# Optimization experiments

Measured on AMD Instinct MI355X. Metric: run time of the kernel, lower is better.

## Reference

```python
import jax, jax.numpy as jnp
import numpy as np

KERNEL_SIZES = [2, 4, 8, 16, 32, 64]
MAXK = max(k + k // 2 for k in KERNEL_SIZES[1:])  # 96
PAD_LO = (MAXK - 1) // 2  # 47
PAD_HI = MAXK - 1 - PAD_LO  # 48


def _alternating(K, even_negative):
    f = np.ones(K, np.float32)
    idx = np.arange(K)
    mask = (idx % 2 == 0) if even_negative else (idx % 2 == 1)
    f[mask] = -1.0
    return f


def make_weight_bank():
    """Builds all 17 fixed filters, zero-padded and center-aligned into one
    (17, 1, MAXK) bank so a single 'same'-padded conv matches 17 torch convs.
    Alignment: torch pads left=(K-1)//2 for kernel K; embedding each kernel at
    offset (MAXK-1)//2 - (K-1)//2 inside a MAXK kernel padded (PAD_LO, PAD_HI)
    reproduces the identical output."""
    filters = []
    for K in KERNEL_SIZES:              # group 1: -1 at even indices
        filters.append(_alternating(K, True))
    for K in KERNEL_SIZES:              # group 2: -1 at odd indices
        filters.append(_alternating(K, False))
    for K in KERNEL_SIZES[1:]:          # group 3: piecewise quadratic, len K + K//2
        q = K // 4
        left = (np.linspace(0.0, 1.0, q + 1, dtype=np.float32)[1:]) ** 2
        right = left[::-1]
        filters.append(np.concatenate([-left, -right, 2 * left, 2 * right, -left, -right]).astype(np.float32))
    W = np.zeros((len(filters), 1, MAXK), np.float32)
    for i, f in enumerate(filters):
        K = len(f)
        o = (MAXK - 1) // 2 - (K - 1) // 2
        W[i, 0, o:o + K] = f
    return jnp.asarray(W)


def setup_inputs() -> dict:
    key = jax.random.key(0)
    x = jax.random.normal(key, (128, 1, 32768), dtype=jnp.float32)
    W = make_weight_bank()  # (17, 1, 96), fixed non-trainable filters
    return {"x": x, "W": W}


def reference(x, W):
    # x: (B, 1, L); W: (17, 1, MAXK). One cross-correlation conv = bank of 17
    # 'same'-padded conv1d filters; then ReLU.
    y = jax.lax.conv_general_dilated(
        x, W,
        window_strides=(1,),
        padding=[(PAD_LO, PAD_HI)],
        dimension_numbers=("NCH", "OIH", "NCH"),
    )
    return jax.nn.relu(y)  # (B, 17, L)
```

## Files before the change

### kernel.cpp

```cpp
#include <hip/hip_runtime.h>


#define S_LEN   32768
#define NFILT   17
#define TILE    1024
#define HALO_L  47
#define WIN     (TILE + 96)
#define NCHUNK  (WIN / 8)
#define PITCH   284
#define NTHREADS 256

template<int Q>
__device__ __forceinline__ float third_w(int j) {
    constexpr float inv = 1.0f / (float)Q;
    const int seg = j / Q;
    const int i = j - seg * Q;
    const float t = (seg == 0 || seg == 2 || seg == 4) ? (float)(i + 1) * inv
                                                       : (float)(Q - i) * inv;
    const float v = t * t;
    return (seg == 2 || seg == 3) ? 2.0f * v : -v;
}

template<int K>
__device__ __forceinline__ float4 third_acc(const float* __restrict__ xsp, int tid) {
    constexpr int Q    = K / 4;
    constexpr int SPAN = 6 * Q;
    constexpr int C    = (3 * K / 2 - 1) / 2;
    float a0 = 0.f, a1 = 0.f, a2 = 0.f, a3 = 0.f;
#pragma unroll
    for (int u = 0; u < SPAN + 3; ++u) {
        const int d = (HALO_L - C) + u;
        const float xv = xsp[(d & 3) * PITCH + tid + (d >> 2)];
        if (u < SPAN)               a0 = fmaf(third_w<Q>(u),     xv, a0);
        if (u >= 1 && u - 1 < SPAN) a1 = fmaf(third_w<Q>(u - 1), xv, a1);
        if (u >= 2 && u - 2 < SPAN) a2 = fmaf(third_w<Q>(u - 2), xv, a2);
        if (u >= 3 && u - 3 < SPAN) a3 = fmaf(third_w<Q>(u - 3), xv, a3);
    }
    return make_float4(a0, a1, a2, a3);
}

template<int K>
__device__ __forceinline__ float4 alt_acc(const float* __restrict__ Qsp, int tid) {
    constexpr int H = (K - 1) / 2;
    float v[4];
#pragma unroll
    for (int r = 0; r < 4; ++r) {
        const int d  = HALO_L + r - H;
        const int d2 = d + K;
        const float qa = Qsp[(d  & 3) * PITCH + tid + (d  >> 2)];
        const float qb = Qsp[(d2 & 3) * PITCH + tid + (d2 >> 2)];
        const float dd = qb - qa;
        v[r] = (d & 1) ? dd : -dd;
    }
    return make_float4(v[0], v[1], v[2], v[3]);
}

__global__ __launch_bounds__(NTHREADS)
void conv_bank_kernel(const float* __restrict__ x, float* __restrict__ out) {
    __shared__ float xsp[4 * PITCH];
    __shared__ float Qsp[4 * PITCH];
    __shared__ float scanb[NTHREADS];

    const int tid = threadIdx.x;
    const int ts  = blockIdx.x * TILE;
    const int b   = blockIdx.y;
    const float* __restrict__ xrow = x + (size_t)b * S_LEN;

    for (int j = tid; j < WIN; j += NTHREADS) {
        const int g = ts - HALO_L + j;
        float v = 0.f;
        if ((unsigned)g < (unsigned)S_LEN) v = xrow[g];
        xsp[(j & 3) * PITCH + (j >> 2)] = v;
    }
    __syncthreads();

    float csum = 0.f;
    if (tid < NCHUNK) {
#pragma unroll
        for (int k = 0; k < 8; ++k) {
            const float v = xsp[(k & 3) * PITCH + 2 * tid + (k >> 2)];
            csum += (k & 1) ? -v : v;
        }
    }
    scanb[tid] = csum;
    __syncthreads();
    float incl = csum;
#pragma unroll
    for (int off = 1; off < NTHREADS; off <<= 1) {
        const float add = (tid >= off) ? scanb[tid - off] : 0.f;
        __syncthreads();
        incl += add;
        scanb[tid] = incl;
        __syncthreads();
    }
    if (tid < NCHUNK) {
        float run = incl - csum;
#pragma unroll
        for (int k = 0; k < 8; ++k) {
            const int idx = (k & 3) * PITCH + 2 * tid + (k >> 2);
            Qsp[idx] = run;
            const float v = xsp[idx];
            run += (k & 1) ? -v : v;
        }
        if (tid == NCHUNK - 1) Qsp[WIN >> 2] = run;
    }
    __syncthreads();

    const int t0 = ts + 4 * tid;
    float* __restrict__ obase = out + (size_t)b * NFILT * S_LEN + t0;

    auto store_relu = [&](int j, float4 v) {
        float4 s;
        s.x = fmaxf(v.x, 0.f); s.y = fmaxf(v.y, 0.f);
        s.z = fmaxf(v.z, 0.f); s.w = fmaxf(v.w, 0.f);
        *reinterpret_cast<float4*>(obase + (size_t)j * S_LEN) = s;
    };
    auto store_pair = [&](int j, float4 a) {
        store_relu(j, a);
        store_relu(j + 6, make_float4(-a.x, -a.y, -a.z, -a.w));
    };

    store_pair(0, alt_acc<2 >(Qsp, tid));
    store_pair(1, alt_acc<4 >(Qsp, tid));
    store_pair(2, alt_acc<8 >(Qsp, tid));
    store_pair(3, alt_acc<16>(Qsp, tid));
    store_pair(4, alt_acc<32>(Qsp, tid));
    store_pair(5, alt_acc<64>(Qsp, tid));

    store_relu(12, third_acc<4 >(xsp, tid));
    store_relu(13, third_acc<8 >(xsp, tid));
    store_relu(14, third_acc<16>(xsp, tid));
    store_relu(15, third_acc<32>(xsp, tid));
    store_relu(16, third_acc<64>(xsp, tid));
}

extern "C" void kernel_launch(void* const* d_in, const int* in_sizes, int n_in,
                              void* d_out, int out_size, void* d_ws, size_t ws_size,
                              hipStream_t stream) {
    const float* x = (const float*)d_in[0];
    float* out = (float*)d_out;
    const int nbatch = in_sizes[0] / S_LEN;
    dim3 grid(S_LEN / TILE, nbatch, 1);
    conv_bank_kernel<<<grid, NTHREADS, 0, stream>>>(x, out);
}
```

Baseline: 297.9 us.

## Factor quadratic filters into shared bump convolutions and use wave-shuffle scan

```diff
diff --git a/kernel.cpp b/kernel.cpp
--- a/kernel.cpp
+++ b/kernel.cpp
@@ -1,113 +1,170 @@
 #include <hip/hip_runtime.h>
 
 
-#define S_LEN   32768
-#define NFILT   17
-#define TILE    1024
-#define HALO_L  47
-#define WIN     (TILE + 96)
-#define NCHUNK  (WIN / 8)
-#define PITCH   284
+#define S_LEN    32768
+#define NFILT    17
+#define TILE     1024
 #define NTHREADS 256
-
-template<int Q>
-__device__ __forceinline__ float third_w(int j) {
-    constexpr float inv = 1.0f / (float)Q;
-    const int seg = j / Q;
-    const int i = j - seg * Q;
-    const float t = (seg == 0 || seg == 2 || seg == 4) ? (float)(i + 1) * inv
-                                                       : (float)(Q - i) * inv;
-    const float v = t * t;
-    return (seg == 2 || seg == 3) ? 2.0f * v : -v;
+#define PITCH    284
+#define NCHUNK   139
+
+constexpr int Z1_OFF  = 0;
+constexpr int Z2_OFF  = Z1_OFF  + TILE + 4;
+constexpr int Z4_OFF  = Z2_OFF  + TILE + 8;
+constexpr int Z8_OFF  = Z4_OFF  + TILE + 16;
+constexpr int Z16_OFF = Z8_OFF  + TILE + 32;
+constexpr int ZTOT    = Z16_OFF + TILE + 64;
+
+template<int Qv>
+__device__ __forceinline__ float bw(int i) {
+    constexpr float inv = 1.0f / (float)Qv;
+    const float t = (i < Qv) ? (float)(i + 1) * inv : (float)(2 * Qv - i) * inv;
+    return t * t;
+}
+
+template<int Qv>
+__device__ __forceinline__ void zcalc(const float* __restrict__ xsl,
+                                      float* __restrict__ Zf, int bi) {
+    constexpr int OFF  = 49 - 3 * Qv;
+    constexpr int A0Q  = OFF >> 2;
+    constexpr int SH   = OFF & 3;
+    constexpr int SPAN = 2 * Qv;
+    constexpr int NW   = (SH + SPAN + 3 + 3) >> 2;
+    const float4* __restrict__ xs4 =
+        reinterpret_cast<const float4*>(xsl) + bi + A0Q;
+    float a0 = 0.f, a1 = 0.f, a2 = 0.f, a3 = 0.f;
+#pragma unroll
+    for (int wi = 0; wi < NW; ++wi) {
+        const float4 xw = xs4[wi];
+#pragma unroll
+        for (int e = 0; e < 4; ++e) {
+            const int u = 4 * wi + e - SH;
+            const float xv = (e == 0) ? xw.x : (e == 1) ? xw.y
+                           : (e == 2) ? xw.z : xw.w;
+            if (u >= 0 && u < SPAN)     a0 = fmaf(bw<Qv>(u),     xv, a0);
+            if (u >= 1 && u < SPAN + 1) a1 = fmaf(bw<Qv>(u - 1), xv, a1);
+            if (u >= 2 && u < SPAN + 2) a2 = fmaf(bw<Qv>(u - 2), xv, a2);
+            if (u >= 3 && u < SPAN + 3) a3 = fmaf(bw<Qv>(u - 3), xv, a3);
+        }
+    }
+    reinterpret_cast<float4*>(Zf)[bi] = make_float4(a0, a1, a2, a3);
+}
+
+template<int Qv>
+__device__ __forceinline__ float4 bump_out(const float* __restrict__ Zf, int tid) {
+    const float4* __restrict__ Z4 = reinterpret_cast<const float4*>(Zf);
+    const float4 za = Z4[tid];
+    float4 y;
+    if constexpr (Qv >= 2) {
+        const float4 zb = Z4[tid + (Qv >> 1)];
+        const float4 zc = Z4[tid + Qv];
+        y.x = fmaf(2.f, zb.x, -(za.x + zc.x));
+        y.y = fmaf(2.f, zb.y, -(za.y + zc.y));
+        y.z = fmaf(2.f, zb.z, -(za.z + zc.z));
+        y.w = fmaf(2.f, zb.w, -(za.w + zc.w));
+    } else {
+        const float4 zb = Z4[tid + 1];
+        y.x = fmaf(2.f, za.z, -(za.x + zb.x));
+        y.y = fmaf(2.f, za.w, -(za.y + zb.y));
+        y.z = fmaf(2.f, zb.x, -(za.z + zb.z));
+        y.w = fmaf(2.f, zb.y, -(za.w + zb.w));
+    }
+    return y;
 }
 
 template<int K>
-__device__ __forceinline__ float4 third_acc(const float* __restrict__ xsp, int tid) {
-    constexpr int Q    = K / 4;
-    constexpr int SPAN = 6 * Q;
-    constexpr int C    = (3 * K / 2 - 1) / 2;
-    float a0 = 0.f, a1 = 0.f, a2 = 0.f, a3 = 0.f;
-#pragma unroll
-    for (int u = 0; u < SPAN + 3; ++u) {
-        const int d = (HALO_L - C) + u;
-        const float xv = xsp[(d & 3) * PITCH + tid + (d >> 2)];
-        if (u < SPAN)               a0 = fmaf(third_w<Q>(u),     xv, a0);
-        if (u >= 1 && u - 1 < SPAN) a1 = fmaf(third_w<Q>(u - 1), xv, a1);
-        if (u >= 2 && u - 2 < SPAN) a2 = fmaf(third_w<Q>(u - 2), xv, a2);
-        if (u >= 3 && u - 3 < SPAN) a3 = fmaf(third_w<Q>(u - 3), xv, a3);
-    }
-    return make_float4(a0, a1, a2, a3);
-}
-
-template<int K>
-__device__ __forceinline__ float4 alt_acc(const float* __restrict__ Qsp, int tid) {
+__device__ __forceinline__ float4 alt_acc(const float* __restrict__ Psp, int tid) {
     constexpr int H = (K - 1) / 2;
     float v[4];
 #pragma unroll
     for (int r = 0; r < 4; ++r) {
-        const int d  = HALO_L + r - H;
-        const int d2 = d + K;
-        const float qa = Qsp[(d  & 3) * PITCH + tid + (d  >> 2)];
-        const float qb = Qsp[(d2 & 3) * PITCH + tid + (d2 >> 2)];
-        const float dd = qb - qa;
-        v[r] = (d & 1) ? dd : -dd;
+        const int dn  = 48 - H + r;
+        const int dn2 = dn + K;
+        const float pa = Psp[(dn  & 3) * PITCH + tid + (dn  >> 2)];
+        const float pb = Psp[(dn2 & 3) * PITCH + tid + (dn2 >> 2)];
+        const float dd = pb - pa;
+        v[r] = ((r + H) & 1) ? dd : -dd;
     }
     return make_float4(v[0], v[1], v[2], v[3]);
 }
 
-__global__ __launch_bounds__(NTHREADS)
+__global__ __launch_bounds__(NTHREADS, 4)
 void conv_bank_kernel(const float* __restrict__ x, float* __restrict__ out) {
-    __shared__ float xsp[4 * PITCH];
-    __shared__ float Qsp[4 * PITCH];
-    __shared__ float scanb[NTHREADS];
+    __shared__ __align__(16) float xsl[1136];
+    __shared__ float Psp[4 * PITCH];
+    __shared__ __align__(16) float Zb[ZTOT];
+    __shared__ float wtot[2];
 
     const int tid = threadIdx.x;
-    const int ts  = blockIdx.x * TILE;
+    const int bx  = blockIdx.x;
+    const int ts  = bx * TILE;
     const int b   = blockIdx.y;
     const float* __restrict__ xrow = x + (size_t)b * S_LEN;
 
-    for (int j = tid; j < WIN; j += NTHREADS) {
-        const int g = ts - HALO_L + j;
-        float v = 0.f;
-        if ((unsigned)g < (unsigned)S_LEN) v = xrow[g];
-        xsp[(j & 3) * PITCH + (j >> 2)] = v;
+    if (bx >= 1 && bx <= 30) {
+        const float4* __restrict__ g4 =
+            reinterpret_cast<const float4*>(xrow) + ((ts - 48) >> 2);
+        float4* __restrict__ s4 = reinterpret_cast<float4*>(xsl);
+#pragma unroll
+        for (int i = tid; i < 284; i += NTHREADS)
+            s4[i] = (i < 281) ? g4[i] : make_float4(0.f, 0.f, 0.f, 0.f);
+    } else {
+        for (int j = tid; j < 1136; j += NTHREADS) {
+            const int g = ts - 48 + j;
+            xsl[j] = (j < 1124 && (unsigned)g < (unsigned)S_LEN) ? xrow[g] : 0.f;
+        }
     }
     __syncthreads();
 
-    float csum = 0.f;
+    float4 xa, xb;
+    float csum = 0.f, incl;
+    {
+        const float4* __restrict__ xs4 = reinterpret_cast<const float4*>(xsl);
+        if (tid < NCHUNK) {
+            xa = xs4[2 * tid];
+            xb = xs4[2 * tid + 1];
+            csum = (xa.x - xa.y) + (xa.z - xa.w)
+                 + (xb.x - xb.y) + (xb.z - xb.w);
+        }
+        incl = csum;
+#pragma unroll
+        for (int off = 1; off < 64; off <<= 1) {
+            const float v = __shfl_up(incl, off, 64);
+            if ((tid & 63) >= off) incl += v;
+        }
+        if ((tid & 63) == 63 && tid < 128) wtot[tid >> 6] = incl;
+    }
+    zcalc<16>(xsl, Zb + Z16_OFF, tid);
+    zcalc<8 >(xsl, Zb + Z8_OFF,  tid);
+    if (tid >= 192 && tid < 208) zcalc<16>(xsl, Zb + Z16_OFF, 256 + (tid - 192));
+    if (tid >= 208 && tid < 216) zcalc<8 >(xsl, Zb + Z8_OFF,  256 + (tid - 208));
+    __syncthreads();
+
+    zcalc<4>(xsl, Zb + Z4_OFF, tid);
+    zcalc<2>(xsl, Zb + Z2_OFF, tid);
+    zcalc<1>(xsl, Zb + Z1_OFF, tid);
+    if (tid >= 216 && tid < 220) zcalc<4>(xsl, Zb + Z4_OFF, 256 + (tid - 216));
+    if (tid >= 220 && tid < 222) zcalc<2>(xsl, Zb + Z2_OFF, 256 + (tid - 220));
+    if (tid == 222)              zcalc<1>(xsl, Zb + Z1_OFF, 256);
+
     if (tid < NCHUNK) {
-#pragma unroll
-        for (int k = 0; k < 8; ++k) {
-            const float v = xsp[(k & 3) * PITCH + 2 * tid + (k >> 2)];
-            csum += (k & 1) ? -v : v;
-        }
-    }
-    scanb[tid] = csum;
+        float offs = (tid >= 64) ? wtot[0] : 0.f;
+        if (tid >= 128) offs += wtot[1];
+        float run = offs + (incl - csum);
+        float* __restrict__ Pb = Psp + 2 * tid;
+        Pb[0 * PITCH + 0] = run; run += xa.x;
+        Pb[1 * PITCH + 0] = run; run -= xa.y;
+        Pb[2 * PITCH + 0] = run; run += xa.z;
+        Pb[3 * PITCH + 0] = run; run -= xa.w;
+        Pb[0 * PITCH + 1] = run; run += xb.x;
+        Pb[1 * PITCH + 1] = run; run -= xb.y;
+        Pb[2 * PITCH + 1] = run; run += xb.z;
+        Pb[3 * PITCH + 1] = run;
+    }
     __syncthreads();
-    float incl = csum;
-#pragma unroll
-    for (int off = 1; off < NTHREADS; off <<= 1) {
-        const float add = (tid >= off) ? scanb[tid - off] : 0.f;
-        __syncthreads();
-        incl += add;
-        scanb[tid] = incl;
-        __syncthreads();
-    }
-    if (tid < NCHUNK) {
-        float run = incl - csum;
-#pragma unroll
-        for (int k = 0; k < 8; ++k) {
-            const int idx = (k & 3) * PITCH + 2 * tid + (k >> 2);
-            Qsp[idx] = run;
-            const float v = xsp[idx];
-            run += (k & 1) ? -v : v;
-        }
-        if (tid == NCHUNK - 1) Qsp[WIN >> 2] = run;
-    }
-    __syncthreads();
 
     const int t0 = ts + 4 * tid;
-    float* __restrict__ obase = out + (size_t)b * NFILT * S_LEN + t0;
+    float* __restrict__ obase = out + (size_t)b * (NFILT * S_LEN) + t0;
 
     auto store_relu = [&](int j, float4 v) {
         float4 s;
@@ -120,18 +177,18 @@
         store_relu(j + 6, make_float4(-a.x, -a.y, -a.z, -a.w));
     };
 
-    store_pair(0, alt_acc<2 >(Qsp, tid));
-    store_pair(1, alt_acc<4 >(Qsp, tid));
-    store_pair(2, alt_acc<8 >(Qsp, tid));
-    store_pair(3, alt_acc<16>(Qsp, tid));
-    store_pair(4, alt_acc<32>(Qsp, tid));
-    store_pair(5, alt_acc<64>(Qsp, tid));
-
-    store_relu(12, third_acc<4 >(xsp, tid));
-    store_relu(13, third_acc<8 >(xsp, tid));
-    store_relu(14, third_acc<16>(xsp, tid));
-    store_relu(15, third_acc<32>(xsp, tid));
-    store_relu(16, third_acc<64>(xsp, tid));
+    store_pair(0, alt_acc<2 >(Psp, tid));
+    store_pair(1, alt_acc<4 >(Psp, tid));
+    store_pair(2, alt_acc<8 >(Psp, tid));
+    store_pair(3, alt_acc<16>(Psp, tid));
+    store_pair(4, alt_acc<32>(Psp, tid));
+    store_pair(5, alt_acc<64>(Psp, tid));
+
+    store_relu(12, bump_out<1 >(Zb + Z1_OFF,  tid));
+    store_relu(13, bump_out<2 >(Zb + Z2_OFF,  tid));
+    store_relu(14, bump_out<4 >(Zb + Z4_OFF,  tid));
+    store_relu(15, bump_out<8 >(Zb + Z8_OFF,  tid));
+    store_relu(16, bump_out<16>(Zb + Z16_OFF, tid));
 }
 
 extern "C" void kernel_launch(void* const* d_in, const int* in_sizes, int n_in,
```

After: 302.5 us. Within noise of the previous version (+1.5%).
